# Optimization experiments

Hardware: AMD Instinct MI355X
Metric: run time of the kernel (lower is better)

Reference implementation:

```python
import jax, jax.numpy as jnp
import numpy as np
from jax import lax

SEQ, FEAT, U1, U2, U3, OUT = 20, 5, 10, 7, 4, 4
BATCH = 262144


def _he_uniform(key, shape, fan_in):
    lim = np.sqrt(6.0 / fan_in)
    return jax.random.uniform(key, shape, jnp.float32, -lim, lim)


def _orthogonal(key, n, m):
    a = jax.random.normal(key, (max(n, m), min(n, m)), jnp.float32)
    q, _ = jnp.linalg.qr(a)
    return q[:n, :m] if n >= m else q[:m, :n].T


def _lstm_params(key, in_dim, units):
    k1, k2 = jax.random.split(key)
    Wk = _he_uniform(k1, (in_dim, 4 * units), in_dim)
    Wr = _orthogonal(k2, units, 4 * units)
    # Keras unit_forget_bias: bias = [zeros(i), ones(f), zeros(c), zeros(o)]
    b = jnp.concatenate([jnp.zeros(units), jnp.ones(units), jnp.zeros(2 * units)]).astype(jnp.float32)
    return Wk, Wr, b


def setup_inputs() -> dict:
    key = jax.random.key(0)
    ks = jax.random.split(key, 5)
    x = jax.random.normal(ks[0], (BATCH, SEQ, FEAT), jnp.float32)
    Wk1, Wr1, b1 = _lstm_params(ks[1], FEAT, U1)
    Wk2, Wr2, b2 = _lstm_params(ks[2], U1, U2)
    Wk3, Wr3, b3 = _lstm_params(ks[3], U2, U3)
    kd1, kd2 = jax.random.split(ks[4])
    lim = np.sqrt(6.0 / (U3 + OUT))  # glorot_uniform (Dense default)
    Wd = jax.random.uniform(kd1, (U3, OUT), jnp.float32, -lim, lim)
    bd = jnp.zeros((OUT,), jnp.float32)
    return {"x": x, "Wk1": Wk1, "Wr1": Wr1, "b1": b1,
            "Wk2": Wk2, "Wr2": Wr2, "b2": b2,
            "Wk3": Wk3, "Wr3": Wr3, "b3": b3,
            "Wd": Wd, "bd": bd}


def lstm_layer(x, Wk, Wr, b):
    # x: [B, T, F] -> h-sequence [B, T, U]; Keras gate order i, f, c(g), o
    B = x.shape[0]
    U = Wr.shape[0]
    # precompute input projection for all timesteps (one big GEMM)
    zx = jnp.einsum('btf,fg->btg', x, Wk) + b  # [B, T, 4U]
    zxT = jnp.swapaxes(zx, 0, 1)               # [T, B, 4U]

    def step(carry, zt):
        h, c = carry
        z = zt + h @ Wr
        i, f, g, o = jnp.split(z, 4, axis=-1)
        i = jax.nn.sigmoid(i)
        f = jax.nn.sigmoid(f)
        g = jnp.tanh(g)
        o = jax.nn.sigmoid(o)
        c = f * c + i * g
        h = o * jnp.tanh(c)
        return (h, c), h

    init = (jnp.zeros((B, U), x.dtype), jnp.zeros((B, U), x.dtype))
    _, hs = lax.scan(step, init, zxT)
    return jnp.swapaxes(hs, 0, 1)  # [B, T, U]


def reference(x, Wk1, Wr1, b1, Wk2, Wr2, b2, Wk3, Wr3, b3, Wd, bd):
    h = lstm_layer(x, Wk1, Wr1, b1)
    h = lstm_layer(h, Wk2, Wr2, b2)
    h = lstm_layer(h, Wk3, Wr3, b3)
    return jax.nn.sigmoid(jnp.einsum('btu,uo->bto', h, Wd) + bd)
```

## Files before the change

### kernel.cpp

```cpp
#include <hip/hip_runtime.h>

static constexpr int SEQ = 20, FEAT = 5, NU1 = 10, NU2 = 7, NU3 = 4, NOUT = 4;

typedef short bf16x8 __attribute__((ext_vector_type(8)));
typedef float f32x4  __attribute__((ext_vector_type(4)));


static constexpr int WAVE_LDS = 9728;
static constexpr int OFF_L2 = 2816, OFF_L3 = 6144, OFF_D = 8448;

__device__ __forceinline__ unsigned short bf16_hi_rne(float x) {
    unsigned u = __float_as_uint(x);
    return (unsigned short)((u + 0x7FFF + ((u >> 16) & 1)) >> 16);
}
__device__ __forceinline__ unsigned short bf16_trunc(float x) {
    return (unsigned short)(__float_as_uint(x) >> 16);
}
__device__ __forceinline__ float bf16_to_f(unsigned short h) {
    return __uint_as_float(((unsigned)h) << 16);
}
__device__ __forceinline__ unsigned hpack(float h) {
    unsigned u = __float_as_uint(h);
    unsigned r = (u + 0x7FFF + ((u >> 16) & 1)) >> 16;
    unsigned lo = __float_as_uint(h - __uint_as_float(r << 16)) >> 16;
    return r | (lo << 16);
}

__device__ __forceinline__ float sigm(float x) {
    return __builtin_amdgcn_rcpf(1.0f + __builtin_amdgcn_exp2f(x * -1.4426950408889634f));
}
__device__ __forceinline__ float ftanh(float x) {
    return 1.0f - 2.0f * __builtin_amdgcn_rcpf(1.0f + __builtin_amdgcn_exp2f(x * 2.8853900817779268f));
}

__device__ __forceinline__ unsigned act_unit(const f32x4 z, float& c) {
    float gi = sigm(z[0]), gf = sigm(z[1]), gg = ftanh(z[2]), go = sigm(z[3]);
    c = gf * c + gi * gg;
    return hpack(go * ftanh(c));
}

__global__ void build_afrags(const float* Wk1, const float* Wr1, const float* b1,
                             const float* Wk2, const float* Wr2, const float* b2,
                             const float* Wk3, const float* Wr3, const float* b3,
                             const float* Wd,  const float* bd, unsigned* ws) {
    const int lane = threadIdx.x;
    const int Us[3] = {NU1, NU2, NU3}, Is[3] = {15, 17, 11}, Ss[3] = {5, 10, 7};
    const float* Wa[3] = {Wk1, Wk2, Wk3};
    const float* Wb[3] = {Wr1, Wr2, Wr3};
    const float* bs[3] = {b1, b2, b3};
    const int baseid[3] = {0, 6, 12}, KT[3] = {2, 3, 2}, MT[3] = {3, 2, 1};
    for (int L = 0; L < 3; ++L) {
        const int U = Us[L], I = Is[L], Sp = Ss[L];
        for (int tau = 0; tau < MT[L]; ++tau)
        for (int kap = 0; kap < KT[L]; ++kap) {
            const int id = baseid[L] + tau * KT[L] + kap;
            unsigned short h8[8];
            for (int j = 0; j < 8; ++j) {
                const int m = lane & 15;
                const int k = kap * 32 + (lane >> 4) * 8 + j;
                const int i = k >> 2, cls = k & 3;
                const int u = tau * 4 + (m >> 2), g = m & 3, col = g * U + u;
                unsigned short v = 0;
                if (u < U) {
                    if (i < I) {
                        float W = (i < Sp) ? Wa[L][i * 4 * U + col]
                                           : Wb[L][(i - Sp) * 4 * U + col];
                        unsigned short hi = bf16_hi_rne(W);
                        v = (cls < 2) ? hi : bf16_trunc(W - bf16_to_f(hi));
                    } else if (i == I) {
                        float bv = bs[L][col];
                        unsigned short hi = bf16_hi_rne(bv);
                        v = (cls == 0) ? hi : ((cls == 1) ? bf16_trunc(bv - bf16_to_f(hi)) : (unsigned short)0);
                    }
                }
                h8[j] = v;
            }
            for (int d = 0; d < 4; ++d)
                ws[id * 256 + lane * 4 + d] = (unsigned)h8[2 * d] | ((unsigned)h8[2 * d + 1] << 16);
        }
    }
    {
        unsigned short h8[8];
        for (int j = 0; j < 8; ++j) {
            const int m = lane & 15;
            const int k = (lane >> 4) * 8 + j;
            const int i = k >> 2, cls = k & 3;
            unsigned short v = 0;
            if (m < NOUT) {
                if (i < 4) {
                    float W = Wd[i * NOUT + m];
                    unsigned short hi = bf16_hi_rne(W);
                    v = (cls < 2) ? hi : bf16_trunc(W - bf16_to_f(hi));
                } else if (i == 4) {
                    float bv = bd[m];
                    unsigned short hi = bf16_hi_rne(bv);
                    v = (cls == 0) ? hi : ((cls == 1) ? bf16_trunc(bv - bf16_to_f(hi)) : (unsigned short)0);
                }
            }
            h8[j] = v;
        }
        for (int d = 0; d < 4; ++d)
            ws[14 * 256 + lane * 4 + d] = (unsigned)h8[2 * d] | ((unsigned)h8[2 * d + 1] << 16);
    }
}

__global__ __launch_bounds__(256, 3) void lstm3_mfma(
    const float* __restrict__ x, const unsigned* __restrict__ wsA,
    float* __restrict__ out, int B) {
    __shared__ __attribute__((aligned(16))) char lds_raw[4 * WAVE_LDS];
    const int tid = threadIdx.x;
    const int lane = tid & 63;
    const int n = lane & 15;
    const int q = lane >> 4;
    char* S  = lds_raw + (tid >> 6) * WAVE_LDS;
    char* L1 = S;
    char* L2 = S + OFF_L2;
    char* L3 = S + OFF_L3;
    char* SD = S + OFF_D;

    bf16x8 af[15];
#pragma unroll
    for (int i = 0; i < 15; ++i) {
        uint4 v = ((const uint4*)wsA)[i * 64 + lane];
        af[i] = __builtin_bit_cast(bf16x8, v);
    }

    char* rB1 = L1 + n * 176 + 16 * q;
    char* rB2 = L2 + n * 208 + 16 * q;
    char* rB3 = L3 + n * 144 + 16 * q;
    char* rBD = SD + n * 64 + 16 * q;
    char* wL1s = L1 + n * 176 + 40 + 8 * q;
    char* wL2a = L2 + n * 208 + 8 * q;
    char* wL2s = L2 + n * 208 + 80 + 8 * q;
    char* wL3a = L3 + n * 144 + 8 * q;
    char* wL3s = L3 + n * 144 + 56 + 8 * q;
    char* wDa  = SD + n * 64 + 8 * q;
    char* wx1  = L1 + (lane >> 2) * 176 + 8 * (lane & 3);
    char* wx2  = L1 + lane * 176 + 32;

    const int ngrp = B >> 4;
    const int gw = (blockIdx.x * blockDim.x + tid) >> 6;
    const int nw = (gridDim.x * blockDim.x) >> 6;

    for (int grp = gw; grp < ngrp; grp += nw) {
#pragma unroll
        for (int i = 0; i < 9; ++i) *(uint4*)(S + i * 1024 + lane * 16) = uint4{0, 0, 0, 0};
        if (lane < 32) *(uint4*)(S + 9 * 1024 + lane * 16) = uint4{0, 0, 0, 0};
        if (lane < 16) {
            *(unsigned*)(L1 + lane * 176 + 120) = 0x3F803F80u;
            *(unsigned*)(L2 + lane * 208 + 136) = 0x3F803F80u;
            *(unsigned*)(L3 + lane * 144 + 88)  = 0x3F803F80u;
            *(unsigned*)(SD + lane * 64 + 32)   = 0x3F803F80u;
        }

        float c10 = 0.f, c11 = 0.f, c12 = 0.f, c20 = 0.f, c21 = 0.f, c30 = 0.f;
        const float* xb = x + (size_t)grp * 16 * (SEQ * FEAT);
        float* ob = out + (size_t)grp * 16 * (SEQ * NOUT);

#pragma unroll 1
        for (int t = 0; t < SEQ; ++t) {
            {
                float xv = xb[(lane >> 2) * 100 + t * 5 + (lane & 3)];
                unsigned p = hpack(xv);
                *(uint2*)wx1 = uint2{p, p};
                if (lane < 16) {
                    float x4 = xb[lane * 100 + t * 5 + 4];
                    unsigned p2 = hpack(x4);
                    *(uint2*)wx2 = uint2{p2, p2};
                }
            }
            bf16x8 b0 = *(const bf16x8*)(rB1);
            bf16x8 b1v = *(const bf16x8*)(rB1 + 64);
            f32x4 z0 = {0, 0, 0, 0}, z1 = {0, 0, 0, 0}, z2 = {0, 0, 0, 0};
            z0 = __builtin_amdgcn_mfma_f32_16x16x32_bf16(af[0], b0,  z0, 0, 0, 0);
            z0 = __builtin_amdgcn_mfma_f32_16x16x32_bf16(af[1], b1v, z0, 0, 0, 0);
            z1 = __builtin_amdgcn_mfma_f32_16x16x32_bf16(af[2], b0,  z1, 0, 0, 0);
            z1 = __builtin_amdgcn_mfma_f32_16x16x32_bf16(af[3], b1v, z1, 0, 0, 0);
            z2 = __builtin_amdgcn_mfma_f32_16x16x32_bf16(af[4], b0,  z2, 0, 0, 0);
            z2 = __builtin_amdgcn_mfma_f32_16x16x32_bf16(af[5], b1v, z2, 0, 0, 0);
            {
                unsigned p = act_unit(z0, c10);
                *(uint2*)(wL1s + 0) = uint2{p, p};
                *(uint2*)(wL2a + 0) = uint2{p, p};
                p = act_unit(z1, c11);
                *(uint2*)(wL1s + 32) = uint2{p, p};
                *(uint2*)(wL2a + 32) = uint2{p, p};
                p = act_unit(z2, c12);
                if (q < 2) {
                    *(uint2*)(wL1s + 64) = uint2{p, p};
                    *(uint2*)(wL2a + 64) = uint2{p, p};
                }
            }
            bf16x8 c0 = *(const bf16x8*)(rB2);
            bf16x8 c1v = *(const bf16x8*)(rB2 + 64);
            bf16x8 c2v = *(const bf16x8*)(rB2 + 128);
            f32x4 y0 = {0, 0, 0, 0}, y1 = {0, 0, 0, 0};
            y0 = __builtin_amdgcn_mfma_f32_16x16x32_bf16(af[6],  c0,  y0, 0, 0, 0);
            y0 = __builtin_amdgcn_mfma_f32_16x16x32_bf16(af[7],  c1v, y0, 0, 0, 0);
            y0 = __builtin_amdgcn_mfma_f32_16x16x32_bf16(af[8],  c2v, y0, 0, 0, 0);
            y1 = __builtin_amdgcn_mfma_f32_16x16x32_bf16(af[9],  c0,  y1, 0, 0, 0);
            y1 = __builtin_amdgcn_mfma_f32_16x16x32_bf16(af[10], c1v, y1, 0, 0, 0);
            y1 = __builtin_amdgcn_mfma_f32_16x16x32_bf16(af[11], c2v, y1, 0, 0, 0);
            {
                unsigned p = act_unit(y0, c20);
                *(uint2*)(wL2s + 0) = uint2{p, p};
                *(uint2*)(wL3a + 0) = uint2{p, p};
                p = act_unit(y1, c21);
                if (q < 3) {
                    *(uint2*)(wL2s + 32) = uint2{p, p};
                    *(uint2*)(wL3a + 32) = uint2{p, p};
                }
            }
            bf16x8 d0v = *(const bf16x8*)(rB3);
            bf16x8 d1v = *(const bf16x8*)(rB3 + 64);
            f32x4 w0 = {0, 0, 0, 0};
            w0 = __builtin_amdgcn_mfma_f32_16x16x32_bf16(af[12], d0v, w0, 0, 0, 0);
            w0 = __builtin_amdgcn_mfma_f32_16x16x32_bf16(af[13], d1v, w0, 0, 0, 0);
            {
                unsigned p = act_unit(w0, c30);
                *(uint2*)wL3s = uint2{p, p};
                *(uint2*)wDa  = uint2{p, p};
            }
            bf16x8 e0 = *(const bf16x8*)(rBD);
            f32x4 o0 = {0, 0, 0, 0};
            o0 = __builtin_amdgcn_mfma_f32_16x16x32_bf16(af[14], e0, o0, 0, 0, 0);
            if (lane < 16) {
                float4 o4;
                o4.x = sigm(o0[0]); o4.y = sigm(o0[1]);
                o4.z = sigm(o0[2]); o4.w = sigm(o0[3]);
                *(float4*)(ob + lane * (SEQ * NOUT) + t * NOUT) = o4;
            }
        }
    }
}

extern "C" void kernel_launch(void* const* d_in, const int* in_sizes, int n_in,
                              void* d_out, int out_size, void* d_ws, size_t ws_size,
                              hipStream_t stream) {
    const float* x   = (const float*)d_in[0];
    const float* Wk1 = (const float*)d_in[1];
    const float* Wr1 = (const float*)d_in[2];
    const float* b1  = (const float*)d_in[3];
    const float* Wk2 = (const float*)d_in[4];
    const float* Wr2 = (const float*)d_in[5];
    const float* b2  = (const float*)d_in[6];
    const float* Wk3 = (const float*)d_in[7];
    const float* Wr3 = (const float*)d_in[8];
    const float* b3  = (const float*)d_in[9];
    const float* Wd  = (const float*)d_in[10];
    const float* bd  = (const float*)d_in[11];
    float* out = (float*)d_out;
    unsigned* ws = (unsigned*)d_ws;

    const int B = in_sizes[0] / (SEQ * FEAT);

    build_afrags<<<1, 64, 0, stream>>>(Wk1, Wr1, b1, Wk2, Wr2, b2,
                                       Wk3, Wr3, b3, Wd, bd, ws);
    lstm3_mfma<<<1024, 256, 0, stream>>>(x, ws, out, B);
}
```

Before: 421.7 us.

## Replace LDS staging of MFMA B-fragments with ds_bpermute register shuffles

The per-wave LDS scratch used to stage hidden states and inputs as MFMA B operands is removed. Fragments are now assembled in registers via ds_bpermute lane shuffles, with the K-dimension reordered (recurrent/feed-forward first) and weights repacked to match. The next timestep's x is prefetched into registers. Occupancy is raised (launch bounds 4, grid doubled) now that LDS is gone. This risks correctness through the intricate lane-index mapping and adds more shuffle instructions per step.

```diff
diff --git a/kernel.cpp b/kernel.cpp
--- a/kernel.cpp
+++ b/kernel.cpp
@@ -5,9 +5,6 @@
 typedef short bf16x8 __attribute__((ext_vector_type(8)));
 typedef float f32x4  __attribute__((ext_vector_type(4)));
 
-
-static constexpr int WAVE_LDS = 9728;
-static constexpr int OFF_L2 = 2816, OFF_L3 = 6144, OFF_D = 8448;
 
 __device__ __forceinline__ unsigned short bf16_hi_rne(float x) {
     unsigned u = __float_as_uint(x);
@@ -39,18 +36,29 @@
     return hpack(go * ftanh(c));
 }
 
+__device__ __forceinline__ unsigned bperm(int idx, unsigned v) {
+    return (unsigned)__builtin_amdgcn_ds_bpermute(idx, (int)v);
+}
+__device__ __forceinline__ bf16x8 bfrag(unsigned v0, unsigned v1) {
+    uint4 u{v0, v0, v1, v1};
+    return __builtin_bit_cast(bf16x8, u);
+}
+
 __global__ void build_afrags(const float* Wk1, const float* Wr1, const float* b1,
                              const float* Wk2, const float* Wr2, const float* b2,
                              const float* Wk3, const float* Wr3, const float* b3,
                              const float* Wd,  const float* bd, unsigned* ws) {
     const int lane = threadIdx.x;
-    const int Us[3] = {NU1, NU2, NU3}, Is[3] = {15, 17, 11}, Ss[3] = {5, 10, 7};
-    const float* Wa[3] = {Wk1, Wk2, Wk3};
-    const float* Wb[3] = {Wr1, Wr2, Wr3};
-    const float* bs[3] = {b1, b2, b3};
+    const int Us[3] = {NU1, NU2, NU3};
+    const int nF[3] = {10, 10, 7};
+    const int nS[3] = {5, 7, 4};
+    const float* Fm[3] = {Wr1, Wk2, Wk3};
+    const float* Sm[3] = {Wk1, Wr2, Wr3};
+    const float* Bs[3] = {b1, b2, b3};
     const int baseid[3] = {0, 6, 12}, KT[3] = {2, 3, 2}, MT[3] = {3, 2, 1};
     for (int L = 0; L < 3; ++L) {
-        const int U = Us[L], I = Is[L], Sp = Ss[L];
+        const int U = Us[L], nf = nF[L], ns = nS[L];
+        const int Itot = nf + ns;
         for (int tau = 0; tau < MT[L]; ++tau)
         for (int kap = 0; kap < KT[L]; ++kap) {
             const int id = baseid[L] + tau * KT[L] + kap;
@@ -61,17 +69,12 @@
                 const int i = k >> 2, cls = k & 3;
                 const int u = tau * 4 + (m >> 2), g = m & 3, col = g * U + u;
                 unsigned short v = 0;
-                if (u < U) {
-                    if (i < I) {
-                        float W = (i < Sp) ? Wa[L][i * 4 * U + col]
-                                           : Wb[L][(i - Sp) * 4 * U + col];
-                        unsigned short hi = bf16_hi_rne(W);
-                        v = (cls < 2) ? hi : bf16_trunc(W - bf16_to_f(hi));
-                    } else if (i == I) {
-                        float bv = bs[L][col];
-                        unsigned short hi = bf16_hi_rne(bv);
-                        v = (cls == 0) ? hi : ((cls == 1) ? bf16_trunc(bv - bf16_to_f(hi)) : (unsigned short)0);
-                    }
+                if (u < U && i <= Itot) {
+                    float W = (i < nf)   ? Fm[L][i * 4 * U + col]
+                            : (i < Itot) ? Sm[L][(i - nf) * 4 * U + col]
+                                         : Bs[L][col];
+                    unsigned short hi = bf16_hi_rne(W);
+                    v = (cls < 2) ? hi : bf16_trunc(W - bf16_to_f(hi));
                 }
                 h8[j] = v;
             }
@@ -86,16 +89,10 @@
             const int k = (lane >> 4) * 8 + j;
             const int i = k >> 2, cls = k & 3;
             unsigned short v = 0;
-            if (m < NOUT) {
-                if (i < 4) {
-                    float W = Wd[i * NOUT + m];
-                    unsigned short hi = bf16_hi_rne(W);
-                    v = (cls < 2) ? hi : bf16_trunc(W - bf16_to_f(hi));
-                } else if (i == 4) {
-                    float bv = bd[m];
-                    unsigned short hi = bf16_hi_rne(bv);
-                    v = (cls == 0) ? hi : ((cls == 1) ? bf16_trunc(bv - bf16_to_f(hi)) : (unsigned short)0);
-                }
+            if (m < NOUT && i <= 4) {
+                float W = (i < 4) ? Wd[i * NOUT + m] : bd[m];
+                unsigned short hi = bf16_hi_rne(W);
+                v = (cls < 2) ? hi : bf16_trunc(W - bf16_to_f(hi));
             }
             h8[j] = v;
         }
@@ -104,19 +101,13 @@
     }
 }
 
-__global__ __launch_bounds__(256, 3) void lstm3_mfma(
+__global__ __launch_bounds__(256, 4) void lstm3_mfma(
     const float* __restrict__ x, const unsigned* __restrict__ wsA,
     float* __restrict__ out, int B) {
-    __shared__ __attribute__((aligned(16))) char lds_raw[4 * WAVE_LDS];
     const int tid = threadIdx.x;
     const int lane = tid & 63;
     const int n = lane & 15;
     const int q = lane >> 4;
-    char* S  = lds_raw + (tid >> 6) * WAVE_LDS;
-    char* L1 = S;
-    char* L2 = S + OFF_L2;
-    char* L3 = S + OFF_L3;
-    char* SD = S + OFF_D;
 
     bf16x8 af[15];
 #pragma unroll
@@ -125,110 +116,110 @@
         af[i] = __builtin_bit_cast(bf16x8, v);
     }
 
-    char* rB1 = L1 + n * 176 + 16 * q;
-    char* rB2 = L2 + n * 208 + 16 * q;
-    char* rB3 = L3 + n * 144 + 16 * q;
-    char* rBD = SD + n * 64 + 16 * q;
-    char* wL1s = L1 + n * 176 + 40 + 8 * q;
-    char* wL2a = L2 + n * 208 + 8 * q;
-    char* wL2s = L2 + n * 208 + 80 + 8 * q;
-    char* wL3a = L3 + n * 144 + 8 * q;
-    char* wL3s = L3 + n * 144 + 56 + 8 * q;
-    char* wDa  = SD + n * 64 + 8 * q;
-    char* wx1  = L1 + (lane >> 2) * 176 + 8 * (lane & 3);
-    char* wx2  = L1 + lane * 176 + 32;
+    const int ie  = (n + 16 * ((2 * q) & 3))     << 2;
+    const int io  = (n + 16 * ((2 * q + 1) & 3)) << 2;
+    const int ie2 = (n + 16 * ((2 * q + 2) & 3)) << 2;
+    const int io2 = (n + 16 * ((2 * q + 3) & 3)) << 2;
+    const int in0 = n << 2, in1 = (n + 16) << 2, in2 = (n + 32) << 2;
+
+    const f32x4 zro = {0.f, 0.f, 0.f, 0.f};
 
     const int ngrp = B >> 4;
     const int gw = (blockIdx.x * blockDim.x + tid) >> 6;
     const int nw = (gridDim.x * blockDim.x) >> 6;
 
     for (int grp = gw; grp < ngrp; grp += nw) {
-#pragma unroll
-        for (int i = 0; i < 9; ++i) *(uint4*)(S + i * 1024 + lane * 16) = uint4{0, 0, 0, 0};
-        if (lane < 32) *(uint4*)(S + 9 * 1024 + lane * 16) = uint4{0, 0, 0, 0};
-        if (lane < 16) {
-            *(unsigned*)(L1 + lane * 176 + 120) = 0x3F803F80u;
-            *(unsigned*)(L2 + lane * 208 + 136) = 0x3F803F80u;
-            *(unsigned*)(L3 + lane * 144 + 88)  = 0x3F803F80u;
-            *(unsigned*)(SD + lane * 64 + 32)   = 0x3F803F80u;
-        }
-
+        const float* xr = x + (size_t)grp * 16 * (SEQ * FEAT) + n * (SEQ * FEAT);
+        float* ob = out + (size_t)grp * 16 * (SEQ * NOUT) + n * (SEQ * NOUT);
+
+        unsigned p1a = 0, p1b = 0, p1c = 0, p2a = 0, p2b = 0, p3 = 0;
+        unsigned F0v0 = 0, F0v1 = 0, tC0 = 0, tC1 = 0;
         float c10 = 0.f, c11 = 0.f, c12 = 0.f, c20 = 0.f, c21 = 0.f, c30 = 0.f;
-        const float* xb = x + (size_t)grp * 16 * (SEQ * FEAT);
-        float* ob = out + (size_t)grp * 16 * (SEQ * NOUT);
+
+        float xa = 0.f, xc = 0.f;
+        if (q != 0) {
+            const float* p = xr + 2 * (q - 1);
+            xa = p[0];
+            if (q != 3) xc = p[1];
+        }
 
 #pragma unroll 1
         for (int t = 0; t < SEQ; ++t) {
-            {
-                float xv = xb[(lane >> 2) * 100 + t * 5 + (lane & 3)];
-                unsigned p = hpack(xv);
-                *(uint2*)wx1 = uint2{p, p};
-                if (lane < 16) {
-                    float x4 = xb[lane * 100 + t * 5 + 4];
-                    unsigned p2 = hpack(x4);
-                    *(uint2*)wx2 = uint2{p2, p2};
+            unsigned xP0 = hpack(xa), xP1 = hpack(xc);
+            {
+                const int tn = (t + 1 < SEQ) ? t + 1 : 0;
+                if (q != 0) {
+                    const float* p = xr + tn * FEAT + 2 * (q - 1);
+                    xa = p[0];
+                    if (q != 3) xc = p[1];
                 }
             }
-            bf16x8 b0 = *(const bf16x8*)(rB1);
-            bf16x8 b1v = *(const bf16x8*)(rB1 + 64);
-            f32x4 z0 = {0, 0, 0, 0}, z1 = {0, 0, 0, 0}, z2 = {0, 0, 0, 0};
-            z0 = __builtin_amdgcn_mfma_f32_16x16x32_bf16(af[0], b0,  z0, 0, 0, 0);
-            z0 = __builtin_amdgcn_mfma_f32_16x16x32_bf16(af[1], b1v, z0, 0, 0, 0);
-            z1 = __builtin_amdgcn_mfma_f32_16x16x32_bf16(af[2], b0,  z1, 0, 0, 0);
-            z1 = __builtin_amdgcn_mfma_f32_16x16x32_bf16(af[3], b1v, z1, 0, 0, 0);
-            z2 = __builtin_amdgcn_mfma_f32_16x16x32_bf16(af[4], b0,  z2, 0, 0, 0);
-            z2 = __builtin_amdgcn_mfma_f32_16x16x32_bf16(af[5], b1v, z2, 0, 0, 0);
-            {
-                unsigned p = act_unit(z0, c10);
-                *(uint2*)(wL1s + 0) = uint2{p, p};
-                *(uint2*)(wL2a + 0) = uint2{p, p};
-                p = act_unit(z1, c11);
-                *(uint2*)(wL1s + 32) = uint2{p, p};
-                *(uint2*)(wL2a + 32) = uint2{p, p};
-                p = act_unit(z2, c12);
-                if (q < 2) {
-                    *(uint2*)(wL1s + 64) = uint2{p, p};
-                    *(uint2*)(wL2a + 64) = uint2{p, p};
-                }
-            }
-            bf16x8 c0 = *(const bf16x8*)(rB2);
-            bf16x8 c1v = *(const bf16x8*)(rB2 + 64);
-            bf16x8 c2v = *(const bf16x8*)(rB2 + 128);
-            f32x4 y0 = {0, 0, 0, 0}, y1 = {0, 0, 0, 0};
-            y0 = __builtin_amdgcn_mfma_f32_16x16x32_bf16(af[6],  c0,  y0, 0, 0, 0);
-            y0 = __builtin_amdgcn_mfma_f32_16x16x32_bf16(af[7],  c1v, y0, 0, 0, 0);
-            y0 = __builtin_amdgcn_mfma_f32_16x16x32_bf16(af[8],  c2v, y0, 0, 0, 0);
-            y1 = __builtin_amdgcn_mfma_f32_16x16x32_bf16(af[9],  c0,  y1, 0, 0, 0);
-            y1 = __builtin_amdgcn_mfma_f32_16x16x32_bf16(af[10], c1v, y1, 0, 0, 0);
-            y1 = __builtin_amdgcn_mfma_f32_16x16x32_bf16(af[11], c2v, y1, 0, 0, 0);
-            {
-                unsigned p = act_unit(y0, c20);
-                *(uint2*)(wL2s + 0) = uint2{p, p};
-                *(uint2*)(wL3a + 0) = uint2{p, p};
-                p = act_unit(y1, c21);
-                if (q < 3) {
-                    *(uint2*)(wL2s + 32) = uint2{p, p};
-                    *(uint2*)(wL3a + 32) = uint2{p, p};
-                }
-            }
-            bf16x8 d0v = *(const bf16x8*)(rB3);
-            bf16x8 d1v = *(const bf16x8*)(rB3 + 64);
-            f32x4 w0 = {0, 0, 0, 0};
-            w0 = __builtin_amdgcn_mfma_f32_16x16x32_bf16(af[12], d0v, w0, 0, 0, 0);
-            w0 = __builtin_amdgcn_mfma_f32_16x16x32_bf16(af[13], d1v, w0, 0, 0, 0);
-            {
-                unsigned p = act_unit(w0, c30);
-                *(uint2*)wL3s = uint2{p, p};
-                *(uint2*)wDa  = uint2{p, p};
-            }
-            bf16x8 e0 = *(const bf16x8*)(rBD);
-            f32x4 o0 = {0, 0, 0, 0};
-            o0 = __builtin_amdgcn_mfma_f32_16x16x32_bf16(af[14], e0, o0, 0, 0, 0);
-            if (lane < 16) {
+            unsigned F1v0 = (q == 0) ? tC0 : xP0;
+            unsigned F1v1 = (q == 0) ? tC1 : ((q == 3) ? 0x3F80u : xP1);
+
+            f32x4 z0 = __builtin_amdgcn_mfma_f32_16x16x32_bf16(af[0], bfrag(F0v0, F0v1), zro, 0, 0, 0);
+            z0 = __builtin_amdgcn_mfma_f32_16x16x32_bf16(af[1], bfrag(F1v0, F1v1), z0, 0, 0, 0);
+            f32x4 z1 = __builtin_amdgcn_mfma_f32_16x16x32_bf16(af[2], bfrag(F0v0, F0v1), zro, 0, 0, 0);
+            z1 = __builtin_amdgcn_mfma_f32_16x16x32_bf16(af[3], bfrag(F1v0, F1v1), z1, 0, 0, 0);
+            f32x4 z2 = __builtin_amdgcn_mfma_f32_16x16x32_bf16(af[4], bfrag(F0v0, F0v1), zro, 0, 0, 0);
+            z2 = __builtin_amdgcn_mfma_f32_16x16x32_bf16(af[5], bfrag(F1v0, F1v1), z2, 0, 0, 0);
+            p1a = act_unit(z0, c10);
+            p1b = act_unit(z1, c11);
+            p1c = act_unit(z2, c12);
+
+            {
+                unsigned ae = bperm(ie, p1a), be = bperm(ie, p1b);
+                unsigned ao = bperm(io, p1a), bo = bperm(io, p1b);
+                F0v0 = (q < 2) ? ae : be;
+                F0v1 = (q < 2) ? ao : bo;
+                tC0 = bperm(in0, p1c);
+                tC1 = bperm(in1, p1c);
+            }
+            unsigned F2v0, F2v1, F3v0;
+            {
+                unsigned de = bperm(ie2, p2a), ee = bperm(ie2, p2b);
+                unsigned dd = bperm(io2, p2a), eo = bperm(io2, p2b);
+                F2v0 = (q == 0) ? tC0 : ((q < 3) ? de : ee);
+                F2v1 = (q == 0) ? tC1 : ((q < 3) ? dd : eo);
+                F3v0 = bperm(in2, p2b);
+            }
+            const unsigned F3v1 = 0x3F80u;
+
+            f32x4 y0 = __builtin_amdgcn_mfma_f32_16x16x32_bf16(af[6], bfrag(F0v0, F0v1), zro, 0, 0, 0);
+            y0 = __builtin_amdgcn_mfma_f32_16x16x32_bf16(af[7], bfrag(F2v0, F2v1), y0, 0, 0, 0);
+            y0 = __builtin_amdgcn_mfma_f32_16x16x32_bf16(af[8], bfrag(F3v0, F3v1), y0, 0, 0, 0);
+            f32x4 y1 = __builtin_amdgcn_mfma_f32_16x16x32_bf16(af[9], bfrag(F0v0, F0v1), zro, 0, 0, 0);
+            y1 = __builtin_amdgcn_mfma_f32_16x16x32_bf16(af[10], bfrag(F2v0, F2v1), y1, 0, 0, 0);
+            y1 = __builtin_amdgcn_mfma_f32_16x16x32_bf16(af[11], bfrag(F3v0, F3v1), y1, 0, 0, 0);
+            p2a = act_unit(y0, c20);
+            p2b = act_unit(y1, c21);
+
+            unsigned F4v0, F4v1, F5v0, F5v1;
+            {
+                unsigned ge = bperm(ie, p2a), he = bperm(ie, p2b);
+                unsigned go = bperm(io, p2a), ho = bperm(io, p2b);
+                unsigned pp0 = bperm(in0, p3);
+                F4v0 = (q < 2) ? ge : he;
+                F4v1 = (q < 2) ? go : ((q == 2) ? ho : pp0);
+                F5v0 = bperm(io, p3);
+                F5v1 = (q == 1) ? 0x3F80u : bperm(in2, p3);
+            }
+            f32x4 w0 = __builtin_amdgcn_mfma_f32_16x16x32_bf16(af[12], bfrag(F4v0, F4v1), zro, 0, 0, 0);
+            w0 = __builtin_amdgcn_mfma_f32_16x16x32_bf16(af[13], bfrag(F5v0, F5v1), w0, 0, 0, 0);
+            p3 = act_unit(w0, c30);
+
+            unsigned F6v0, F6v1;
+            {
+                unsigned ue = bperm(ie, p3), uo = bperm(io, p3);
+                F6v0 = (q == 2) ? 0x3F80u : ue;
+                F6v1 = uo;
+            }
+            f32x4 o0 = __builtin_amdgcn_mfma_f32_16x16x32_bf16(af[14], bfrag(F6v0, F6v1), zro, 0, 0, 0);
+            if (q == 0) {
                 float4 o4;
                 o4.x = sigm(o0[0]); o4.y = sigm(o0[1]);
                 o4.z = sigm(o0[2]); o4.w = sigm(o0[3]);
-                *(float4*)(ob + lane * (SEQ * NOUT) + t * NOUT) = o4;
+                *(float4*)(ob + t * NOUT) = o4;
             }
         }
     }
@@ -256,5 +247,5 @@
 
     build_afrags<<<1, 64, 0, stream>>>(Wk1, Wr1, b1, Wk2, Wr2, b2,
                                        Wk3, Wr3, b3, Wd, bd, ws);
-    lstm3_mfma<<<1024, 256, 0, stream>>>(x, ws, out, B);
-}
+    lstm3_mfma<<<2048, 256, 0, stream>>>(x, ws, out, B);
+}
```

New measurement: 392.9 us. -6.8%, faster.
